# Kernel tuning notes

Measured on AMD Instinct MI355X. Metric: run time of the kernel, lower is better.

## Reference

```python
import jax, jax.numpy as jnp
import numpy as np

TOP_K = 8


def setup_inputs() -> dict:
    key = jax.random.key(0)
    k0, k1, k2, k3, k4 = jax.random.split(key, 5)
    B, S, H = 1, 1024, 2048
    E, I = 64, 768
    return {
        "hidden_states": jax.random.normal(k0, (B, S, H), dtype=jnp.float32),
        "gate_w": jax.random.normal(k1, (E, H), dtype=jnp.float32) * 0.02,
        "w1": jax.random.normal(k2, (E, H, I), dtype=jnp.float32) * 0.02,  # gate proj
        "w3": jax.random.normal(k3, (E, H, I), dtype=jnp.float32) * 0.02,  # up proj
        "w2": jax.random.normal(k4, (E, I, H), dtype=jnp.float32) * 0.02,  # down proj
    }


def reference(hidden_states, gate_w, w1, w3, w2):
    B, S, H = hidden_states.shape
    x = hidden_states.reshape(-1, H)                      # [T, H]
    T = x.shape[0]
    E = gate_w.shape[0]

    # --- gating: fp32 logits, softmax over all experts, then top-k ---
    logits = x.astype(jnp.float32) @ gate_w.T             # [T, E]
    probs = jax.nn.softmax(logits, axis=-1)
    topk_w, topk_idx = jax.lax.top_k(probs, TOP_K)        # [T, K]
    # norm_topk_prob renormalization
    topk_w = topk_w / (jnp.sum(topk_w, axis=-1, keepdims=True) + 1e-20)

    # scatter top-k weights into dense [T, E] combine matrix (zeros elsewhere)
    combine_w = jnp.zeros((T, E), dtype=probs.dtype).at[
        jnp.arange(T)[:, None], topk_idx
    ].add(topk_w)                                         # [T, E]

    # --- expert SwiGLU MLPs (dense-masked form of grouped GEMM) ---
    g = jnp.einsum('th,ehi->tei', x, w1)                  # [T, E, I]
    u = jnp.einsum('th,ehi->tei', x, w3)                  # [T, E, I]
    a = jax.nn.silu(g) * u                                # [T, E, I]
    # weighted combine: sum_e combine_w[t,e] * (a[t,e] @ w2[e])
    y = jnp.einsum('te,tei,eih->th', combine_w.astype(x.dtype), a, w2)  # [T, H]
    return y.reshape(B, S, H)
```

## Files before the change

kernel.cpp:

```cpp
#include <hip/hip_runtime.h>
#include <hip/hip_bf16.h>
#include <math.h>

#define TT 1024
#define HH 2048
#define EE 64
#define II 768
#define TOPK 8

#define TM 64
#define TN 64
#define TKH 32
#define APAD 4

__global__ void zero_kernel(float* __restrict__ out, int n_out, int* __restrict__ counts) {
    int i = blockIdx.x * blockDim.x + threadIdx.x;
    if (i < n_out) out[i] = 0.f;
    if (i < EE) counts[i] = 0;
}

__global__ __launch_bounds__(64) void gate_kernel(
    const float* __restrict__ x, const float* __restrict__ gw,
    int* __restrict__ counts, int* __restrict__ list_pair, float* __restrict__ list_wt)
{
    int t = blockIdx.x;
    int e = threadIdx.x;
    const float4* xr = (const float4*)(x + (size_t)t * HH);
    const float4* gr = (const float4*)(gw + (size_t)e * HH);
    float acc = 0.f;
    #pragma unroll 4
    for (int h = 0; h < HH / 4; ++h) {
        float4 a = xr[h], b = gr[h];
        acc += a.x * b.x + a.y * b.y + a.z * b.z + a.w * b.w;
    }
    __shared__ float slog[EE];
    slog[e] = acc;
    __syncthreads();
    if (e == 0) {
        float lv[TOPK];
        int li[TOPK];
        unsigned long long used = 0ULL;
        for (int k = 0; k < TOPK; ++k) {
            float best = -INFINITY;
            int bi = 0;
            for (int j = 0; j < EE; ++j) {
                if (!((used >> j) & 1ULL) && slog[j] > best) { best = slog[j]; bi = j; }
            }
            used |= 1ULL << bi;
            lv[k] = best;
            li[k] = bi;
        }
        float mx = lv[0];
        float w[TOPK];
        float s = 0.f;
        for (int k = 0; k < TOPK; ++k) { w[k] = __expf(lv[k] - mx); s += w[k]; }
        float inv = 1.f / s;
        for (int k = 0; k < TOPK; ++k) {
            int ex = li[k];
            int pos = atomicAdd(&counts[ex], 1);
            list_pair[ex * TT + pos] = t * TOPK + k;
            list_wt[ex * TT + pos] = w[k] * inv;
        }
    }
}

__global__ __launch_bounds__(256) void expert_up_kernel(
    const float* __restrict__ x, const float* __restrict__ w1, const float* __restrict__ w3,
    const int* __restrict__ counts, const int* __restrict__ list_pair, const float* __restrict__ list_wt,
    float* __restrict__ act)
{
    const int e  = blockIdx.x / (II / TN);
    const int nt = blockIdx.x % (II / TN);
    const int n0 = nt * TN;
    const int Ne = counts[e];
    const int tid = threadIdx.x;

    __shared__ alignas(16) float Xs[TKH][TM + APAD];
    __shared__ alignas(16) float W1s[TKH][TN + APAD];
    __shared__ alignas(16) float W3s[TKH][TN + APAD];
    __shared__ int   s_pair[TM];
    __shared__ float s_wt[TM];

    const int mg = tid >> 4;
    const int ng = tid & 15;
    const int mb = mg * 4, nb = ng * 4;

    for (int m0 = 0; m0 < Ne; m0 += TM) {
        if (tid < TM) {
            int m = m0 + tid;
            if (m < Ne) { s_pair[tid] = list_pair[e * TT + m]; s_wt[tid] = list_wt[e * TT + m]; }
            else        { s_pair[tid] = 0;                     s_wt[tid] = 0.f; }
        }
        float accg[4][4] = {{0.f}}, accu[4][4] = {{0.f}};

        for (int k0 = 0; k0 < HH; k0 += TKH) {
            __syncthreads();
            {
                int m  = tid >> 2;
                int kb = (tid & 3) * 8;
                int tok = s_pair[m] >> 3;
                const float* src = x + (size_t)tok * HH + k0 + kb;
                float4 v0 = *(const float4*)(src);
                float4 v1 = *(const float4*)(src + 4);
                Xs[kb + 0][m] = v0.x; Xs[kb + 1][m] = v0.y; Xs[kb + 2][m] = v0.z; Xs[kb + 3][m] = v0.w;
                Xs[kb + 4][m] = v1.x; Xs[kb + 5][m] = v1.y; Xs[kb + 6][m] = v1.z; Xs[kb + 7][m] = v1.w;
            }
            {
                int kk  = tid >> 3;
                int nbb = (tid & 7) * 8;
                size_t off = ((size_t)(e * HH + k0 + kk)) * II + n0 + nbb;
                *(float4*)&W1s[kk][nbb]     = *(const float4*)(w1 + off);
                *(float4*)&W1s[kk][nbb + 4] = *(const float4*)(w1 + off + 4);
                *(float4*)&W3s[kk][nbb]     = *(const float4*)(w3 + off);
                *(float4*)&W3s[kk][nbb + 4] = *(const float4*)(w3 + off + 4);
            }
            __syncthreads();
            #pragma unroll
            for (int kk = 0; kk < TKH; ++kk) {
                float4 a  = *(const float4*)&Xs[kk][mb];
                float4 b1 = *(const float4*)&W1s[kk][nb];
                float4 b3 = *(const float4*)&W3s[kk][nb];
                float av[4]  = {a.x, a.y, a.z, a.w};
                float b1v[4] = {b1.x, b1.y, b1.z, b1.w};
                float b3v[4] = {b3.x, b3.y, b3.z, b3.w};
                #pragma unroll
                for (int i2 = 0; i2 < 4; ++i2)
                    #pragma unroll
                    for (int j = 0; j < 4; ++j) {
                        accg[i2][j] += av[i2] * b1v[j];
                        accu[i2][j] += av[i2] * b3v[j];
                    }
            }
        }
        #pragma unroll
        for (int i2 = 0; i2 < 4; ++i2) {
            int m = mb + i2;
            if (m0 + m < Ne) {
                int p = s_pair[m];
                float wt = s_wt[m];
                float* dst = act + (size_t)p * II + n0 + nb;
                #pragma unroll
                for (int j = 0; j < 4; ++j) {
                    float g = accg[i2][j], u = accu[i2][j];
                    float sg = g / (1.f + __expf(-g));
                    dst[j] = wt * sg * u;
                }
            }
        }
        __syncthreads();
    }
}

#define TKI 32
__global__ __launch_bounds__(256) void expert_down_kernel(
    const float* __restrict__ act, const float* __restrict__ w2,
    const int* __restrict__ counts, const int* __restrict__ list_pair,
    float* __restrict__ out)
{
    const int e  = blockIdx.x / (HH / TN);
    const int nt = blockIdx.x % (HH / TN);
    const int n0 = nt * TN;
    const int Ne = counts[e];
    const int tid = threadIdx.x;

    __shared__ alignas(16) float As[TKI][TM + APAD];
    __shared__ alignas(16) float Bs[TKI][TN + APAD];
    __shared__ int s_pair[TM];

    const int mg = tid >> 4;
    const int ng = tid & 15;
    const int mb = mg * 4, nb = ng * 4;

    for (int m0 = 0; m0 < Ne; m0 += TM) {
        if (tid < TM) {
            int m = m0 + tid;
            s_pair[tid] = (m < Ne) ? list_pair[e * TT + m] : 0;
        }
        float acc[4][4] = {{0.f}};

        for (int k0 = 0; k0 < II; k0 += TKI) {
            __syncthreads();
            {
                int m  = tid >> 2;
                int kb = (tid & 3) * 8;
                int p = s_pair[m];
                const float* src = act + (size_t)p * II + k0 + kb;
                float4 v0 = *(const float4*)(src);
                float4 v1 = *(const float4*)(src + 4);
                As[kb + 0][m] = v0.x; As[kb + 1][m] = v0.y; As[kb + 2][m] = v0.z; As[kb + 3][m] = v0.w;
                As[kb + 4][m] = v1.x; As[kb + 5][m] = v1.y; As[kb + 6][m] = v1.z; As[kb + 7][m] = v1.w;
            }
            {
                int kk  = tid >> 3;
                int nbb = (tid & 7) * 8;
                size_t off = ((size_t)(e * II + k0 + kk)) * HH + n0 + nbb;
                *(float4*)&Bs[kk][nbb]     = *(const float4*)(w2 + off);
                *(float4*)&Bs[kk][nbb + 4] = *(const float4*)(w2 + off + 4);
            }
            __syncthreads();
            #pragma unroll
            for (int kk = 0; kk < TKI; ++kk) {
                float4 a = *(const float4*)&As[kk][mb];
                float4 b = *(const float4*)&Bs[kk][nb];
                float av[4] = {a.x, a.y, a.z, a.w};
                float bv[4] = {b.x, b.y, b.z, b.w};
                #pragma unroll
                for (int i2 = 0; i2 < 4; ++i2)
                    #pragma unroll
                    for (int j = 0; j < 4; ++j)
                        acc[i2][j] += av[i2] * bv[j];
            }
        }
        #pragma unroll
        for (int i2 = 0; i2 < 4; ++i2) {
            int m = mb + i2;
            if (m0 + m < Ne) {
                int tok = s_pair[m] >> 3;
                float* dst = out + (size_t)tok * HH + n0 + nb;
                #pragma unroll
                for (int j = 0; j < 4; ++j)
                    atomicAdd(&dst[j], acc[i2][j]);
            }
        }
        __syncthreads();
    }
}

extern "C" void kernel_launch(void* const* d_in, const int* in_sizes, int n_in,
                              void* d_out, int out_size, void* d_ws, size_t ws_size,
                              hipStream_t stream) {
    const float* x  = (const float*)d_in[0];
    const float* gw = (const float*)d_in[1];
    const float* w1 = (const float*)d_in[2];
    const float* w3 = (const float*)d_in[3];
    const float* w2 = (const float*)d_in[4];
    float* out = (float*)d_out;

    char* ws = (char*)d_ws;
    int*   counts    = (int*)ws;
    int*   list_pair = (int*)(ws + 1024);
    float* list_wt   = (float*)(ws + 1024 + 262144);
    float* act       = (float*)(ws + 1024 + 2 * 262144);

    zero_kernel<<<(TT * HH + 255) / 256, 256, 0, stream>>>(out, TT * HH, counts);
    gate_kernel<<<TT, 64, 0, stream>>>(x, gw, counts, list_pair, list_wt);
    expert_up_kernel<<<EE * (II / TN), 256, 0, stream>>>(x, w1, w3, counts, list_pair, list_wt, act);
    expert_down_kernel<<<EE * (HH / TN), 256, 0, stream>>>(act, w2, counts, list_pair, out);
}
```

Baseline: 2.308 ms.

## Rewrite expert GEMMs with bf16 MFMA and a deterministic per-pair combine

Both expert GEMMs are rewritten as 128x128-tile kernels that convert fp32 operands to bf16 while staging them in shared memory and compute with 16x16x32 bf16 MFMA instructions. Each block now handles a single M tile, and blocks whose tile lies beyond the expert's token count exit early. The down projection writes bf16 partial results per (token, k) pair, and a new combine kernel sums them, replacing the fp32 atomics and the full zeroing of the output. The activation buffer is also stored as bf16. This adds precision loss from bf16 and extra workspace traffic for the partial results.

After: 2.496 ms. +8.1%, slower.

```diff
diff --git a/kernel.cpp b/kernel.cpp
--- a/kernel.cpp
+++ b/kernel.cpp
@@ -7,16 +7,23 @@
 #define EE 64
 #define II 768
 #define TOPK 8
-
-#define TM 64
-#define TN 64
-#define TKH 32
-#define APAD 4
-
-__global__ void zero_kernel(float* __restrict__ out, int n_out, int* __restrict__ counts) {
-    int i = blockIdx.x * blockDim.x + threadIdx.x;
-    if (i < n_out) out[i] = 0.f;
-    if (i < EE) counts[i] = 0;
+#define NPAIR (TT * TOPK)
+
+typedef __attribute__((ext_vector_type(8))) short bfrag;
+typedef __attribute__((ext_vector_type(4))) float ffrag;
+
+__device__ inline unsigned short f2bf(float f) {
+    union { float f; unsigned u; } v; v.f = f;
+    unsigned u = v.u;
+    u += 0x7fffu + ((u >> 16) & 1u);
+    return (unsigned short)(u >> 16);
+}
+__device__ inline unsigned packbf(float a, float b) {
+    return (unsigned)f2bf(a) | ((unsigned)f2bf(b) << 16);
+}
+
+__global__ void zero_counts(int* __restrict__ counts) {
+    counts[threadIdx.x] = 0;
 }
 
 __global__ __launch_bounds__(64) void gate_kernel(
@@ -37,193 +44,245 @@
     slog[e] = acc;
     __syncthreads();
     if (e == 0) {
-        float lv[TOPK];
-        int li[TOPK];
+        float lv[TOPK]; int li[TOPK];
         unsigned long long used = 0ULL;
         for (int k = 0; k < TOPK; ++k) {
-            float best = -INFINITY;
-            int bi = 0;
-            for (int j = 0; j < EE; ++j) {
+            float best = -INFINITY; int bi = 0;
+            for (int j = 0; j < EE; ++j)
                 if (!((used >> j) & 1ULL) && slog[j] > best) { best = slog[j]; bi = j; }
-            }
             used |= 1ULL << bi;
-            lv[k] = best;
-            li[k] = bi;
-        }
-        float mx = lv[0];
-        float w[TOPK];
-        float s = 0.f;
+            lv[k] = best; li[k] = bi;
+        }
+        float mx = lv[0], w[TOPK], s = 0.f;
         for (int k = 0; k < TOPK; ++k) { w[k] = __expf(lv[k] - mx); s += w[k]; }
         float inv = 1.f / s;
         for (int k = 0; k < TOPK; ++k) {
             int ex = li[k];
             int pos = atomicAdd(&counts[ex], 1);
             list_pair[ex * TT + pos] = t * TOPK + k;
-            list_wt[ex * TT + pos] = w[k] * inv;
-        }
-    }
-}
-
-__global__ __launch_bounds__(256) void expert_up_kernel(
+            list_wt[ex * TT + pos]  = w[k] * inv;
+        }
+    }
+}
+
+
+#define UP_NT 6
+#define UP_MT 8
+
+__global__ __launch_bounds__(256, 2) void up_mfma(
     const float* __restrict__ x, const float* __restrict__ w1, const float* __restrict__ w3,
     const int* __restrict__ counts, const int* __restrict__ list_pair, const float* __restrict__ list_wt,
-    float* __restrict__ act)
+    __hip_bfloat16* __restrict__ act)
 {
-    const int e  = blockIdx.x / (II / TN);
-    const int nt = blockIdx.x % (II / TN);
-    const int n0 = nt * TN;
-    const int Ne = counts[e];
+    int bx = blockIdx.x;
+    int e   = bx / (UP_MT * UP_NT);
+    int rem = bx % (UP_MT * UP_NT);
+    int mt = rem / UP_NT, nt = rem % UP_NT;
+    int Ne = counts[e];
+    int m0 = mt * 128;
+    if (m0 >= Ne) return;
+    int n0 = nt * 128;
+
+    __shared__ alignas(16) short Xf[8192];
+    __shared__ alignas(16) short W1f[8192];
+    __shared__ alignas(16) short W3f[8192];
+    __shared__ int   s_pair[128];
+    __shared__ float s_wt[128];
+
     const int tid = threadIdx.x;
-
-    __shared__ alignas(16) float Xs[TKH][TM + APAD];
-    __shared__ alignas(16) float W1s[TKH][TN + APAD];
-    __shared__ alignas(16) float W3s[TKH][TN + APAD];
-    __shared__ int   s_pair[TM];
-    __shared__ float s_wt[TM];
-
-    const int mg = tid >> 4;
-    const int ng = tid & 15;
-    const int mb = mg * 4, nb = ng * 4;
-
-    for (int m0 = 0; m0 < Ne; m0 += TM) {
-        if (tid < TM) {
-            int m = m0 + tid;
-            if (m < Ne) { s_pair[tid] = list_pair[e * TT + m]; s_wt[tid] = list_wt[e * TT + m]; }
-            else        { s_pair[tid] = 0;                     s_wt[tid] = 0.f; }
-        }
-        float accg[4][4] = {{0.f}}, accu[4][4] = {{0.f}};
-
-        for (int k0 = 0; k0 < HH; k0 += TKH) {
-            __syncthreads();
-            {
-                int m  = tid >> 2;
-                int kb = (tid & 3) * 8;
-                int tok = s_pair[m] >> 3;
-                const float* src = x + (size_t)tok * HH + k0 + kb;
-                float4 v0 = *(const float4*)(src);
-                float4 v1 = *(const float4*)(src + 4);
-                Xs[kb + 0][m] = v0.x; Xs[kb + 1][m] = v0.y; Xs[kb + 2][m] = v0.z; Xs[kb + 3][m] = v0.w;
-                Xs[kb + 4][m] = v1.x; Xs[kb + 5][m] = v1.y; Xs[kb + 6][m] = v1.z; Xs[kb + 7][m] = v1.w;
-            }
-            {
-                int kk  = tid >> 3;
-                int nbb = (tid & 7) * 8;
-                size_t off = ((size_t)(e * HH + k0 + kk)) * II + n0 + nbb;
-                *(float4*)&W1s[kk][nbb]     = *(const float4*)(w1 + off);
-                *(float4*)&W1s[kk][nbb + 4] = *(const float4*)(w1 + off + 4);
-                *(float4*)&W3s[kk][nbb]     = *(const float4*)(w3 + off);
-                *(float4*)&W3s[kk][nbb + 4] = *(const float4*)(w3 + off + 4);
-            }
-            __syncthreads();
-            #pragma unroll
-            for (int kk = 0; kk < TKH; ++kk) {
-                float4 a  = *(const float4*)&Xs[kk][mb];
-                float4 b1 = *(const float4*)&W1s[kk][nb];
-                float4 b3 = *(const float4*)&W3s[kk][nb];
-                float av[4]  = {a.x, a.y, a.z, a.w};
-                float b1v[4] = {b1.x, b1.y, b1.z, b1.w};
-                float b3v[4] = {b3.x, b3.y, b3.z, b3.w};
+    const int lane = tid & 63;
+    const int w = tid >> 6;
+    const int wm = (w & 1) * 64, wn = (w >> 1) * 64;
+
+    if (tid < 128) {
+        int m = m0 + tid;
+        s_pair[tid] = (m < Ne) ? list_pair[e * TT + m] : 0;
+        s_wt[tid]   = (m < Ne) ? list_wt[e * TT + m]   : 0.f;
+    }
+
+    ffrag accg[4][4], accu[4][4];
+    #pragma unroll
+    for (int i = 0; i < 4; ++i)
+        #pragma unroll
+        for (int j = 0; j < 4; ++j) { accg[i][j] = (ffrag)0.f; accu[i][j] = (ffrag)0.f; }
+
+    for (int k0 = 0; k0 < HH; k0 += 64) {
+        __syncthreads();
+        {
+            int m = tid >> 1, c = tid & 1;
+            int tok = s_pair[m] >> 3;
+            const float* src = x + (size_t)tok * HH + k0 + c * 32;
+            int mtile = m >> 4, mlane = m & 15;
+            #pragma unroll
+            for (int r = 0; r < 8; ++r) {
+                int k = c * 32 + r * 4;
+                float4 v = *(const float4*)(src + r * 4);
+                int s = k >> 5, q = (k >> 3) & 3, j = k & 7;
+                int slot = ((mtile * 2 + s) * 64 + mlane + q * 16) * 8 + j;
+                *(uint2*)&Xf[slot] = make_uint2(packbf(v.x, v.y), packbf(v.z, v.w));
+            }
+        }
+        {
+            int n = tid & 127, kp2 = tid >> 7;
+            int ntile = n >> 4, nl = n & 15;
+            const float* s1 = w1 + ((size_t)e * HH + k0 + kp2 * 32) * II + n0 + n;
+            const float* s3 = w3 + ((size_t)e * HH + k0 + kp2 * 32) * II + n0 + n;
+            #pragma unroll
+            for (int r = 0; r < 16; ++r) {
+                int kp = kp2 * 16 + r;
+                int k = kp * 2;
+                float a1 = s1[(size_t)(2 * r) * II],     b1 = s1[(size_t)(2 * r + 1) * II];
+                float a3 = s3[(size_t)(2 * r) * II],     b3 = s3[(size_t)(2 * r + 1) * II];
+                int s = k >> 5, q = (k >> 3) & 3;
+                int slot = ((ntile * 2 + s) * 64 + nl + q * 16) * 8 + (kp & 3) * 2;
+                *(unsigned*)&W1f[slot] = packbf(a1, b1);
+                *(unsigned*)&W3f[slot] = packbf(a3, b3);
+            }
+        }
+        __syncthreads();
+        #pragma unroll
+        for (int s = 0; s < 2; ++s) {
+            bfrag a[4];
+            #pragma unroll
+            for (int mi = 0; mi < 4; ++mi)
+                a[mi] = *(const bfrag*)&Xf[(((wm >> 4) + mi) * 2 + s) * 64 * 8 + lane * 8];
+            #pragma unroll
+            for (int ni = 0; ni < 4; ++ni) {
+                bfrag b1 = *(const bfrag*)&W1f[(((wn >> 4) + ni) * 2 + s) * 64 * 8 + lane * 8];
+                bfrag b3 = *(const bfrag*)&W3f[(((wn >> 4) + ni) * 2 + s) * 64 * 8 + lane * 8];
                 #pragma unroll
-                for (int i2 = 0; i2 < 4; ++i2)
-                    #pragma unroll
-                    for (int j = 0; j < 4; ++j) {
-                        accg[i2][j] += av[i2] * b1v[j];
-                        accu[i2][j] += av[i2] * b3v[j];
-                    }
-            }
-        }
-        #pragma unroll
-        for (int i2 = 0; i2 < 4; ++i2) {
-            int m = mb + i2;
+                for (int mi = 0; mi < 4; ++mi) {
+                    accg[mi][ni] = __builtin_amdgcn_mfma_f32_16x16x32_bf16(a[mi], b1, accg[mi][ni], 0, 0, 0);
+                    accu[mi][ni] = __builtin_amdgcn_mfma_f32_16x16x32_bf16(a[mi], b3, accu[mi][ni], 0, 0, 0);
+                }
+            }
+        }
+    }
+    int qr = lane >> 4, cl = lane & 15;
+    #pragma unroll
+    for (int mi = 0; mi < 4; ++mi) {
+        #pragma unroll
+        for (int r = 0; r < 4; ++r) {
+            int m = wm + mi * 16 + qr * 4 + r;
             if (m0 + m < Ne) {
                 int p = s_pair[m];
                 float wt = s_wt[m];
-                float* dst = act + (size_t)p * II + n0 + nb;
+                __hip_bfloat16* dst = act + (size_t)p * II + n0;
                 #pragma unroll
-                for (int j = 0; j < 4; ++j) {
-                    float g = accg[i2][j], u = accu[i2][j];
+                for (int ni = 0; ni < 4; ++ni) {
+                    int n = wn + ni * 16 + cl;
+                    float g = accg[mi][ni][r], u = accu[mi][ni][r];
                     float sg = g / (1.f + __expf(-g));
-                    dst[j] = wt * sg * u;
+                    dst[n] = __float2bfloat16(wt * sg * u);
                 }
             }
         }
+    }
+}
+
+#define DN_NT 16
+#define DN_MT 8
+
+__global__ __launch_bounds__(256, 2) void down_mfma(
+    const __hip_bfloat16* __restrict__ act, const float* __restrict__ w2,
+    const int* __restrict__ counts, const int* __restrict__ list_pair,
+    __hip_bfloat16* __restrict__ yp)
+{
+    int bx = blockIdx.x;
+    int e   = bx / (DN_MT * DN_NT);
+    int rem = bx % (DN_MT * DN_NT);
+    int mt = rem / DN_NT, nt = rem % DN_NT;
+    int Ne = counts[e];
+    int m0 = mt * 128;
+    if (m0 >= Ne) return;
+    int n0 = nt * 128;
+
+    __shared__ alignas(16) short Af[8192];
+    __shared__ alignas(16) short Bf[8192];
+    __shared__ int s_pair[128];
+
+    const int tid = threadIdx.x;
+    const int lane = tid & 63;
+    const int w = tid >> 6;
+    const int wm = (w & 1) * 64, wn = (w >> 1) * 64;
+
+    if (tid < 128) {
+        int m = m0 + tid;
+        s_pair[tid] = (m < Ne) ? list_pair[e * TT + m] : 0;
+    }
+
+    ffrag acc[4][4];
+    #pragma unroll
+    for (int i = 0; i < 4; ++i)
+        #pragma unroll
+        for (int j = 0; j < 4; ++j) acc[i][j] = (ffrag)0.f;
+
+    for (int k0 = 0; k0 < II; k0 += 64) {
         __syncthreads();
-    }
-}
-
-#define TKI 32
-__global__ __launch_bounds__(256) void expert_down_kernel(
-    const float* __restrict__ act, const float* __restrict__ w2,
-    const int* __restrict__ counts, const int* __restrict__ list_pair,
-    float* __restrict__ out)
-{
-    const int e  = blockIdx.x / (HH / TN);
-    const int nt = blockIdx.x % (HH / TN);
-    const int n0 = nt * TN;
-    const int Ne = counts[e];
-    const int tid = threadIdx.x;
-
-    __shared__ alignas(16) float As[TKI][TM + APAD];
-    __shared__ alignas(16) float Bs[TKI][TN + APAD];
-    __shared__ int s_pair[TM];
-
-    const int mg = tid >> 4;
-    const int ng = tid & 15;
-    const int mb = mg * 4, nb = ng * 4;
-
-    for (int m0 = 0; m0 < Ne; m0 += TM) {
-        if (tid < TM) {
-            int m = m0 + tid;
-            s_pair[tid] = (m < Ne) ? list_pair[e * TT + m] : 0;
-        }
-        float acc[4][4] = {{0.f}};
-
-        for (int k0 = 0; k0 < II; k0 += TKI) {
-            __syncthreads();
-            {
-                int m  = tid >> 2;
-                int kb = (tid & 3) * 8;
+        #pragma unroll
+        for (int r = 0; r < 4; ++r) {
+            int sidx = r * 256 + tid;
+            int lf = sidx & 63, ss = (sidx >> 6) & 1, mtile = sidx >> 7;
+            int m = mtile * 16 + (lf & 15), q = lf >> 4;
+            int p = s_pair[m];
+            *(uint4*)&Af[sidx * 8] =
+                *(const uint4*)(act + (size_t)p * II + k0 + ss * 32 + q * 8);
+        }
+        {
+            int n = tid & 127, kp2 = tid >> 7;
+            int ntile = n >> 4, nl = n & 15;
+            const float* s2 = w2 + ((size_t)e * II + k0 + kp2 * 32) * HH + n0 + n;
+            #pragma unroll
+            for (int r = 0; r < 16; ++r) {
+                int kp = kp2 * 16 + r;
+                int k = kp * 2;
+                float va = s2[(size_t)(2 * r) * HH], vb = s2[(size_t)(2 * r + 1) * HH];
+                int s = k >> 5, q = (k >> 3) & 3;
+                int slot = ((ntile * 2 + s) * 64 + nl + q * 16) * 8 + (kp & 3) * 2;
+                *(unsigned*)&Bf[slot] = packbf(va, vb);
+            }
+        }
+        __syncthreads();
+        #pragma unroll
+        for (int s = 0; s < 2; ++s) {
+            bfrag a[4];
+            #pragma unroll
+            for (int mi = 0; mi < 4; ++mi)
+                a[mi] = *(const bfrag*)&Af[(((wm >> 4) + mi) * 2 + s) * 64 * 8 + lane * 8];
+            #pragma unroll
+            for (int ni = 0; ni < 4; ++ni) {
+                bfrag b = *(const bfrag*)&Bf[(((wn >> 4) + ni) * 2 + s) * 64 * 8 + lane * 8];
+                #pragma unroll
+                for (int mi = 0; mi < 4; ++mi)
+                    acc[mi][ni] = __builtin_amdgcn_mfma_f32_16x16x32_bf16(a[mi], b, acc[mi][ni], 0, 0, 0);
+            }
+        }
+    }
+    int qr = lane >> 4, cl = lane & 15;
+    #pragma unroll
+    for (int mi = 0; mi < 4; ++mi) {
+        #pragma unroll
+        for (int r = 0; r < 4; ++r) {
+            int m = wm + mi * 16 + qr * 4 + r;
+            if (m0 + m < Ne) {
                 int p = s_pair[m];
-                const float* src = act + (size_t)p * II + k0 + kb;
-                float4 v0 = *(const float4*)(src);
-                float4 v1 = *(const float4*)(src + 4);
-                As[kb + 0][m] = v0.x; As[kb + 1][m] = v0.y; As[kb + 2][m] = v0.z; As[kb + 3][m] = v0.w;
-                As[kb + 4][m] = v1.x; As[kb + 5][m] = v1.y; As[kb + 6][m] = v1.z; As[kb + 7][m] = v1.w;
-            }
-            {
-                int kk  = tid >> 3;
-                int nbb = (tid & 7) * 8;
-                size_t off = ((size_t)(e * II + k0 + kk)) * HH + n0 + nbb;
-                *(float4*)&Bs[kk][nbb]     = *(const float4*)(w2 + off);
-                *(float4*)&Bs[kk][nbb + 4] = *(const float4*)(w2 + off + 4);
-            }
-            __syncthreads();
-            #pragma unroll
-            for (int kk = 0; kk < TKI; ++kk) {
-                float4 a = *(const float4*)&As[kk][mb];
-                float4 b = *(const float4*)&Bs[kk][nb];
-                float av[4] = {a.x, a.y, a.z, a.w};
-                float bv[4] = {b.x, b.y, b.z, b.w};
+                __hip_bfloat16* dst = yp + (size_t)p * HH + n0;
                 #pragma unroll
-                for (int i2 = 0; i2 < 4; ++i2)
-                    #pragma unroll
-                    for (int j = 0; j < 4; ++j)
-                        acc[i2][j] += av[i2] * bv[j];
-            }
-        }
-        #pragma unroll
-        for (int i2 = 0; i2 < 4; ++i2) {
-            int m = mb + i2;
-            if (m0 + m < Ne) {
-                int tok = s_pair[m] >> 3;
-                float* dst = out + (size_t)tok * HH + n0 + nb;
-                #pragma unroll
-                for (int j = 0; j < 4; ++j)
-                    atomicAdd(&dst[j], acc[i2][j]);
-            }
-        }
-        __syncthreads();
-    }
+                for (int ni = 0; ni < 4; ++ni)
+                    dst[wn + ni * 16 + cl] = __float2bfloat16(acc[mi][ni][r]);
+            }
+        }
+    }
+}
+
+__global__ void combine_kernel(const __hip_bfloat16* __restrict__ yp, float* __restrict__ out) {
+    int i = blockIdx.x * blockDim.x + threadIdx.x;
+    int t = i >> 11, h = i & (HH - 1);
+    const __hip_bfloat16* p = yp + (size_t)(t * TOPK) * HH + h;
+    float s = 0.f;
+    #pragma unroll
+    for (int j = 0; j < TOPK; ++j) s += __bfloat162float(p[(size_t)j * HH]);
+    out[i] = s;
 }
 
 extern "C" void kernel_launch(void* const* d_in, const int* in_sizes, int n_in,
@@ -240,10 +299,13 @@
     int*   counts    = (int*)ws;
     int*   list_pair = (int*)(ws + 1024);
     float* list_wt   = (float*)(ws + 1024 + 262144);
-    float* act       = (float*)(ws + 1024 + 2 * 262144);
-
-    zero_kernel<<<(TT * HH + 255) / 256, 256, 0, stream>>>(out, TT * HH, counts);
+    __hip_bfloat16* act = (__hip_bfloat16*)(ws + 1024 + 2 * 262144);
+    __hip_bfloat16* yp  = (__hip_bfloat16*)(ws + 1024 + 2 * 262144 +
+                                            (size_t)NPAIR * II * 2);
+
+    zero_counts<<<1, EE, 0, stream>>>(counts);
     gate_kernel<<<TT, 64, 0, stream>>>(x, gw, counts, list_pair, list_wt);
-    expert_up_kernel<<<EE * (II / TN), 256, 0, stream>>>(x, w1, w3, counts, list_pair, list_wt, act);
-    expert_down_kernel<<<EE * (HH / TN), 256, 0, stream>>>(act, w2, counts, list_pair, out);
-}
+    up_mfma<<<EE * UP_MT * UP_NT, 256, 0, stream>>>(x, w1, w3, counts, list_pair, list_wt, act);
+    down_mfma<<<EE * DN_MT * DN_NT, 256, 0, stream>>>(act, w2, counts, list_pair, yp);
+    combine_kernel<<<(TT * HH) / 256, 256, 0, stream>>>(yp, out);
+}
```
